# Kernel tuning notes

Hardware: AMD Instinct MI355X
Metric: run time of the kernel (lower is better)

The kernel has to match this reference:

```python
import jax, jax.numpy as jnp
import numpy as np

IN_CH = 256
MED_CH = IN_CH // 2


def setup_inputs() -> dict:
    key = jax.random.key(0)
    ks = jax.random.split(key, 9)
    B, C, H, W = 16, IN_CH, 64, 64
    s = 1.0 / np.sqrt(C)
    sm = 1.0 / np.sqrt(MED_CH)
    return {
        "x": jax.random.normal(ks[0], (B, C, H, W), dtype=jnp.float32),
        "w_o": jax.random.normal(ks[1], (MED_CH, C), dtype=jnp.float32) * s,
        "b_o": jax.random.normal(ks[2], (MED_CH,), dtype=jnp.float32) * 0.01,
        "w_v": jax.random.normal(ks[3], (MED_CH, C), dtype=jnp.float32) * s,
        "b_v": jax.random.normal(ks[4], (MED_CH,), dtype=jnp.float32) * 0.01,
        "w_c": jax.random.normal(ks[5], (C, MED_CH), dtype=jnp.float32) * sm,
        "b_c": jax.random.normal(ks[6], (C,), dtype=jnp.float32) * 0.01,
        "gamma": jax.random.normal(ks[7], (1,), dtype=jnp.float32) * 0.1,
    }


def reference(x, w_o, b_o, w_v, b_v, w_c, b_c, gamma):
    B, C, H, W = x.shape
    N = H * W
    xf = x.reshape(B, C, N)  # [B,C,N]
    # 1x1 convs == per-pixel linear projections
    o = jnp.einsum("mc,bcn->bmn", w_o, xf) + b_o[None, :, None]   # [B,M,N]
    v = jnp.einsum("mc,bcn->bmn", w_v, xf) + b_v[None, :, None]   # [B,M,N]
    x_o = o.transpose(0, 2, 1)                                     # [B,N,M]
    x_v = jax.nn.softmax(v, axis=-1)                               # softmax over N
    # NOTE: original code reuses conv_v for the 's' branch (conv_s unused)
    x_s = jax.nn.softmax(v.transpose(0, 2, 1), axis=-1)            # [B,N,M], softmax over M
    A = jnp.einsum("bmn,bnk->bmk", x_v, x_s)                       # [B,M,M]
    Bt = jnp.einsum("bnm,bmk->bnk", x_o, A).transpose(0, 2, 1)     # [B,M,N]
    out = jax.nn.relu(jnp.einsum("cm,bmn->bcn", w_c, Bt) + b_c[None, :, None])
    result = gamma[0] * out.reshape(B, C, H, W) + x
    return result
```

## Files before the change

kernel.cpp:

```cpp
#include <hip/hip_runtime.h>
#include <math.h>

constexpr int Bn = 16;
constexpr int Cn = 256;
constexpr int Mn = 128;
constexpr int Nn = 4096;

typedef short bf16x8 __attribute__((ext_vector_type(8)));
typedef float f32x4 __attribute__((ext_vector_type(4)));
typedef unsigned short us8 __attribute__((ext_vector_type(8)));
typedef unsigned short us4 __attribute__((ext_vector_type(4)));

static __device__ __forceinline__ unsigned short f2bf(float f) {
  union { float f; unsigned int u; } c{f};
  unsigned int u = c.u;
  u += 0x7FFFu + ((u >> 16) & 1u);
  return (unsigned short)(u >> 16);
}

static __device__ __forceinline__ void gload_lds16(const void* g, void* l) {
  __builtin_amdgcn_global_load_lds(
      (const __attribute__((address_space(1))) unsigned int*)g,
      (__attribute__((address_space(3))) unsigned int*)l, 16, 0, 0);
}

__global__ __launch_bounds__(256) void k_prep_w(
    const float* __restrict__ w_o, const float* __restrict__ w_v,
    unsigned short* __restrict__ Wv, unsigned short* __restrict__ woT,
    float* __restrict__ rs) {
  int idx = blockIdx.x * 256 + threadIdx.x;
  if (idx < Bn * Mn) rs[idx] = 0.f;
  if (idx < 8192) {
    int row = idx >> 6;
    int c4 = (idx & 63) * 4;
    float4 f = *(const float4*)&w_v[(size_t)row * Cn + c4];
    us4 g = {f2bf(f.x), f2bf(f.y), f2bf(f.z), f2bf(f.w)};
    *(us4*)&Wv[(size_t)row * Cn + c4] = g;
  } else {
    int j = idx - 8192;
    int cp = j >> 5;
    int m4 = (j & 31) * 4;
    us4 g;
#pragma unroll
    for (int e = 0; e < 4; ++e) g[e] = f2bf(w_o[(size_t)(m4 + e) * Cn + cp]);
    *(us4*)&woT[(size_t)cp * Mn + m4] = g;
  }
}

__global__ __launch_bounds__(256) void k_prep_x(
    const float* __restrict__ x, unsigned short* __restrict__ xT) {
  const int b = blockIdx.z;
  const int c0 = blockIdx.y * 128;
  const int n0 = blockIdx.x * 64;
  const int t = threadIdx.x;
  const int n4 = (t & 15) * 4;
  const int c8 = c0 + (t >> 4) * 8;
  const float* xb = x + ((size_t)b * Cn + c8) * Nn + n0 + n4;
  float4 r[8];
#pragma unroll
  for (int i = 0; i < 8; ++i) r[i] = *(const float4*)&xb[(size_t)i * Nn];
  unsigned short* dst = xT + ((size_t)b * Nn + n0 + n4) * Cn + c8;
#pragma unroll
  for (int j = 0; j < 4; ++j) {
    us8 g;
#pragma unroll
    for (int i = 0; i < 8; ++i) g[i] = f2bf(((const float*)&r[i])[j]);
    *(us8*)&dst[(size_t)j * Cn] = g;
  }
}

__global__ __launch_bounds__(256) void k_proj_v(
    const unsigned short* __restrict__ Wv,
    const unsigned short* __restrict__ xT,
    const float* __restrict__ b_v,
    float* __restrict__ Ap, float* __restrict__ rs) {
  __shared__ us8 pool[16 * 128 * 2];
  __shared__ float cs_lds[4][128];
  unsigned short* ldsA = (unsigned short*)pool;
  unsigned short* ldsB = (unsigned short*)pool + 8 * 128 * 8;
  const int b = blockIdx.y;
  const int nt = blockIdx.x;
  const int t = threadIdx.x;
  const int wave = t >> 6, lane = t & 63;
  const int quad = lane >> 4, l16 = lane & 15;
  const int wm = (wave & 1) * 64, wn = (wave >> 1) * 64;
  f32x4 acc[4][4] = {};
  const unsigned short* xb = xT + ((size_t)b * Nn + nt * 128) * Cn;
  const int rowS = t & 127;
  const int gS = t >> 7;

  uint4 rB[4];
#pragma unroll
  for (int p = 0; p < 4; ++p)
    rB[p] = *(const uint4*)&xb[(size_t)rowS * Cn + (p * 2 + gS) * 8];

  for (int k0 = 0; k0 < Cn; k0 += 64) {
#pragma unroll
    for (int p = 0; p < 4; ++p) {
      int s = p * 256 + t;
      *(uint4*)&ldsB[(size_t)s * 8] = rB[p];
      gload_lds16(&Wv[(size_t)rowS * Cn + k0 + (p * 2 + gS) * 8],
                  &ldsA[(size_t)s * 8]);
    }
    __syncthreads();
    if (k0 + 64 < Cn) {
#pragma unroll
      for (int p = 0; p < 4; ++p)
        rB[p] = *(const uint4*)&xb[(size_t)rowS * Cn + k0 + 64 + (p * 2 + gS) * 8];
    }
#pragma unroll
    for (int s = 0; s < 2; ++s) {
      bf16x8 af[4], bfr[4];
#pragma unroll
      for (int i = 0; i < 4; ++i)
        af[i] = *(const bf16x8*)&ldsA[(size_t)((s * 4 + quad) * 128 + wm + i * 16 + l16) * 8];
#pragma unroll
      for (int j = 0; j < 4; ++j)
        bfr[j] = *(const bf16x8*)&ldsB[(size_t)((s * 4 + quad) * 128 + wn + j * 16 + l16) * 8];
#pragma unroll
      for (int i = 0; i < 4; ++i)
#pragma unroll
        for (int j = 0; j < 4; ++j)
          acc[i][j] = __builtin_amdgcn_mfma_f32_16x16x32_bf16(af[i], bfr[j], acc[i][j], 0, 0, 0);
    }
    __syncthreads();
  }

#pragma unroll
  for (int i = 0; i < 4; ++i) {
#pragma unroll
    for (int r = 0; r < 4; ++r) {
      float bi = b_v[wm + i * 16 + quad * 4 + r];
#pragma unroll
      for (int j = 0; j < 4; ++j)
        acc[i][j][r] = __expf(acc[i][j][r] + bi);
    }
  }

#pragma unroll
  for (int i = 0; i < 4; ++i) {
#pragma unroll
    for (int r = 0; r < 4; ++r) {
      float s = acc[i][0][r] + acc[i][1][r] + acc[i][2][r] + acc[i][3][r];
      s += __shfl_xor(s, 1); s += __shfl_xor(s, 2);
      s += __shfl_xor(s, 4); s += __shfl_xor(s, 8);
      if (l16 == 0)
        atomicAdd(&rs[b * Mn + wm + i * 16 + quad * 4 + r], s);
    }
  }

  float csj[4];
#pragma unroll
  for (int j = 0; j < 4; ++j) {
    float c = 0.f;
#pragma unroll
    for (int i = 0; i < 4; ++i)
#pragma unroll
      for (int r = 0; r < 4; ++r) c += acc[i][j][r];
    c += __shfl_xor(c, 16);
    c += __shfl_xor(c, 32);
    csj[j] = c;
  }
  if (quad == 0) {
#pragma unroll
    for (int j = 0; j < 4; ++j) cs_lds[wave][wn + j * 16 + l16] = csj[j];
  }
  __syncthreads();

  const int cbase = (wave >> 1) * 2;
  float rinv[4];
#pragma unroll
  for (int j = 0; j < 4; ++j) {
    int nl = wn + j * 16 + l16;
    rinv[j] = rsqrtf(cs_lds[cbase][nl] + cs_lds[cbase + 1][nl]);
  }

  unsigned short* Hs = (unsigned short*)pool;
  unsigned short* Ls = Hs + 16 * 128 * 8;
#pragma unroll
  for (int i = 0; i < 4; ++i) {
#pragma unroll
    for (int r = 0; r < 4; ++r) {
      int m = wm + i * 16 + quad * 4 + r;
#pragma unroll
      for (int j = 0; j < 4; ++j) {
        int nl = wn + j * 16 + l16;
        float u = acc[i][j][r] * rinv[j];
        unsigned short h = f2bf(u);
        union { unsigned int q; float f; } hf{(unsigned int)h << 16};
        int idx = ((nl >> 3) * 128 + (m ^ (nl >> 3))) * 8 + (nl & 7);
        Hs[idx] = h;
        Ls[idx] = f2bf(u - hf.f);
      }
    }
  }
  __syncthreads();

  const bf16x8* Hv = (const bf16x8*)pool;
  const bf16x8* Lv = Hv + 16 * 128;
#pragma unroll
  for (int i = 0; i < 4; ++i)
#pragma unroll
    for (int j = 0; j < 4; ++j) acc[i][j] = (f32x4){0.f, 0.f, 0.f, 0.f};
#pragma unroll
  for (int s = 0; s < 4; ++s) {
    int g = s * 4 + quad;
    bf16x8 hA[4], lA[4], hB[4], lB[4];
#pragma unroll
    for (int i = 0; i < 4; ++i) {
      int mi = wm + i * 16 + l16;
      int ki = wn + i * 16 + l16;
      hA[i] = Hv[g * 128 + (mi ^ g)];
      lA[i] = Lv[g * 128 + (mi ^ g)];
      hB[i] = Hv[g * 128 + (ki ^ g)];
      lB[i] = Lv[g * 128 + (ki ^ g)];
    }
#pragma unroll
    for (int i = 0; i < 4; ++i)
#pragma unroll
      for (int j = 0; j < 4; ++j) {
        acc[i][j] = __builtin_amdgcn_mfma_f32_16x16x32_bf16(hA[i], hB[j], acc[i][j], 0, 0, 0);
        acc[i][j] = __builtin_amdgcn_mfma_f32_16x16x32_bf16(hA[i], lB[j], acc[i][j], 0, 0, 0);
        acc[i][j] = __builtin_amdgcn_mfma_f32_16x16x32_bf16(lA[i], hB[j], acc[i][j], 0, 0, 0);
      }
  }

  float* Apb = Ap + ((size_t)nt * Bn + b) * (Mn * Mn);
#pragma unroll
  for (int i = 0; i < 4; ++i) {
#pragma unroll
    for (int r = 0; r < 4; ++r) {
      int m = wm + i * 16 + quad * 4 + r;
      float* row = &Apb[(size_t)m * Mn];
#pragma unroll
      for (int j = 0; j < 4; ++j)
        row[wn + j * 16 + l16] = acc[i][j][r];
    }
  }
}

__global__ __launch_bounds__(256) void k_reduceA(
    const float* __restrict__ Ap, const float* __restrict__ rs,
    float* __restrict__ A, int S) {
  int tid = blockIdx.x * 256 + threadIdx.x;
  int idx4 = tid * 4;
  int b = idx4 / (Mn * Mn);
  int off = idx4 - b * (Mn * Mn);
  float4 s = {0.f, 0.f, 0.f, 0.f};
  for (int s0 = 0; s0 < S; ++s0) {
    float4 p = *(const float4*)&Ap[((size_t)s0 * Bn + b) * (Mn * Mn) + off];
    s.x += p.x; s.y += p.y; s.z += p.z; s.w += p.w;
  }
  float sc = 1.0f / rs[b * Mn + (off >> 7)];
  s.x *= sc; s.y *= sc; s.z *= sc; s.w *= sc;
  *(float4*)&A[idx4] = s;
}

__global__ __launch_bounds__(256) void k_w2(
    const float* __restrict__ w_c, const float* __restrict__ A,
    unsigned short* __restrict__ W2bf) {
  __shared__ float As[64][68];
  __shared__ float wcs[64][68];
  const int b = blockIdx.z;
  const int m0 = blockIdx.x * 64;
  const int c0 = blockIdx.y * 64;
  const int t = threadIdx.x;
  const int tc = (t >> 4) * 4, tmm = (t & 15) * 4;
  float acc[4][4] = {};
  for (int k0 = 0; k0 < Mn; k0 += 64) {
    int r = t >> 2;
    int k4 = (t & 3) * 4;
#pragma unroll
    for (int p = 0; p < 4; ++p) {
      int k = k4 + p * 16;
      float4 a4 = *(const float4*)&A[((size_t)(b * Mn + m0 + r)) * Mn + k0 + k];
      As[k + 0][r] = a4.x; As[k + 1][r] = a4.y; As[k + 2][r] = a4.z; As[k + 3][r] = a4.w;
      float4 w4 = *(const float4*)&w_c[(size_t)(c0 + r) * Mn + k0 + k];
      wcs[k + 0][r] = w4.x; wcs[k + 1][r] = w4.y; wcs[k + 2][r] = w4.z; wcs[k + 3][r] = w4.w;
    }
    __syncthreads();
#pragma unroll
    for (int kk = 0; kk < 64; ++kk) {
      float4 w4 = *(const float4*)&wcs[kk][tc];
      float4 a4 = *(const float4*)&As[kk][tmm];
      float w[4] = {w4.x, w4.y, w4.z, w4.w};
      float a[4] = {a4.x, a4.y, a4.z, a4.w};
#pragma unroll
      for (int i = 0; i < 4; ++i)
#pragma unroll
        for (int jj = 0; jj < 4; ++jj) acc[i][jj] = fmaf(w[i], a[jj], acc[i][jj]);
    }
    __syncthreads();
  }
#pragma unroll
  for (int i = 0; i < 4; ++i) {
    us4 g4 = {f2bf(acc[i][0]), f2bf(acc[i][1]), f2bf(acc[i][2]), f2bf(acc[i][3])};
    *(us4*)&W2bf[((size_t)(b * Cn + c0 + tc + i)) * Mn + m0 + tmm] = g4;
  }
}

__global__ __launch_bounds__(256) void k_ww(
    const unsigned short* __restrict__ W2bf, const unsigned short* __restrict__ woT,
    const float* __restrict__ b_o, const float* __restrict__ b_c,
    unsigned short* __restrict__ WW, float* __restrict__ bb) {
  __shared__ us8 ldsA[128 * 16];
  __shared__ us8 ldsB[128 * 16];
  __shared__ float bo_lds[128];
  const int b = blockIdx.z;
  const int c_t = blockIdx.y * 128;
  const int cp_t = blockIdx.x * 128;
  const int t = threadIdx.x;
  const int wave = t >> 6, lane = t & 63;
  const int quad = lane >> 4, l16 = lane & 15;
  const int wc = (wave & 1) * 64, wp = (wave >> 1) * 64;
  const unsigned short* W2b = W2bf + ((size_t)b * Cn + c_t) * Mn;
  const unsigned short* woB = woT + (size_t)cp_t * Mn;

#pragma unroll
  for (int p = 0; p < 8; ++p) {
    int s = p * 256 + t;
    int row = s >> 4, g = s & 15;
    int slot = row * 16 + (g ^ (row & 15));
    ldsA[slot] = *(const us8*)&W2b[(size_t)row * Mn + g * 8];
    ldsB[slot] = *(const us8*)&woB[(size_t)row * Mn + g * 8];
  }
  if (blockIdx.x == 0 && t < 128) bo_lds[t] = b_o[t];
  __syncthreads();

  f32x4 acc[4][4] = {};
#pragma unroll
  for (int s = 0; s < 4; ++s) {
    int gq = s * 4 + quad;
    int xo = gq ^ l16;
    bf16x8 af[4], bfr[4];
#pragma unroll
    for (int i = 0; i < 4; ++i)
      af[i] = *(const bf16x8*)&ldsA[(wc + i * 16 + l16) * 16 + xo];
#pragma unroll
    for (int j = 0; j < 4; ++j)
      bfr[j] = *(const bf16x8*)&ldsB[(wp + j * 16 + l16) * 16 + xo];
#pragma unroll
    for (int i = 0; i < 4; ++i)
#pragma unroll
      for (int j = 0; j < 4; ++j)
        acc[i][j] = __builtin_amdgcn_mfma_f32_16x16x32_bf16(af[i], bfr[j], acc[i][j], 0, 0, 0);
  }

#pragma unroll
  for (int i = 0; i < 4; ++i) {
#pragma unroll
    for (int r = 0; r < 4; ++r) {
      int c = c_t + wc + i * 16 + quad * 4 + r;
      unsigned short* row = &WW[((size_t)b * Cn + c) * Cn + cp_t];
#pragma unroll
      for (int j = 0; j < 4; ++j)
        row[wp + j * 16 + l16] = f2bf(acc[i][j][r]);
    }
  }

  if (blockIdx.x == 0 && t < 128) {
    float s = 0.f;
#pragma unroll
    for (int g = 0; g < 16; ++g) {
      us8 h = ldsA[t * 16 + (g ^ (t & 15))];
#pragma unroll
      for (int e = 0; e < 8; ++e) {
        union { unsigned int u; float f; } cv{(unsigned int)h[e] << 16};
        s = fmaf(cv.f, bo_lds[g * 8 + e], s);
      }
    }
    bb[b * Cn + c_t + t] = s + b_c[c_t + t];
  }
}

__global__ __launch_bounds__(256) void k_final_mfma(
    const unsigned short* __restrict__ WW, const unsigned short* __restrict__ xT,
    const float* __restrict__ x, const float* __restrict__ bb,
    const float* __restrict__ gamma, float* __restrict__ out) {
  __shared__ us8 ldsA[128 * 16];
  __shared__ us8 ldsB[128 * 16];
  const int b = blockIdx.z;
  const int c_t = blockIdx.y * 128;
  const int n_t = blockIdx.x * 128;
  const int t = threadIdx.x;
  const int wave = t >> 6, lane = t & 63;
  const int quad = lane >> 4, l16 = lane & 15;
  const int wc = (wave & 1) * 64, wn = (wave >> 1) * 64;
  const unsigned short* WWb = WW + ((size_t)b * Cn + c_t) * Cn;
  const unsigned short* xTb = xT + ((size_t)b * Nn + n_t) * Cn;

  f32x4 acc[4][4] = {};
  for (int k0 = 0; k0 < Cn; k0 += 128) {
#pragma unroll
    for (int p = 0; p < 8; ++p) {
      int s = p * 256 + t;
      int row = s >> 4, g = s & 15;
      int slot = row * 16 + (g ^ (row & 15));
      ldsA[slot] = *(const us8*)&WWb[(size_t)row * Cn + k0 + g * 8];
      ldsB[slot] = *(const us8*)&xTb[(size_t)row * Cn + k0 + g * 8];
    }
    __syncthreads();
#pragma unroll
    for (int s = 0; s < 4; ++s) {
      int gq = s * 4 + quad;
      int xo = gq ^ l16;
      bf16x8 af[4], bfr[4];
#pragma unroll
      for (int i = 0; i < 4; ++i)
        af[i] = *(const bf16x8*)&ldsA[(wc + i * 16 + l16) * 16 + xo];
#pragma unroll
      for (int j = 0; j < 4; ++j)
        bfr[j] = *(const bf16x8*)&ldsB[(wn + j * 16 + l16) * 16 + xo];
#pragma unroll
      for (int i = 0; i < 4; ++i)
#pragma unroll
        for (int j = 0; j < 4; ++j)
          acc[i][j] = __builtin_amdgcn_mfma_f32_16x16x32_bf16(af[i], bfr[j], acc[i][j], 0, 0, 0);
    }
    __syncthreads();
  }

  float g = gamma[0];
#pragma unroll
  for (int i = 0; i < 4; ++i) {
#pragma unroll
    for (int r = 0; r < 4; ++r) {
      int c = c_t + wc + i * 16 + quad * 4 + r;
      float bias = bb[b * Cn + c];
      const float* xr = &x[((size_t)b * Cn + c) * Nn + n_t];
      float* orow = &out[((size_t)b * Cn + c) * Nn + n_t];
#pragma unroll
      for (int j = 0; j < 4; ++j) {
        int n = wn + j * 16 + l16;
        orow[n] = g * fmaxf(acc[i][j][r] + bias, 0.f) + xr[n];
      }
    }
  }
}

extern "C" void kernel_launch(void* const* d_in, const int* in_sizes, int n_in,
                              void* d_out, int out_size, void* d_ws, size_t ws_size,
                              hipStream_t stream) {
  const float* x   = (const float*)d_in[0];
  const float* w_o = (const float*)d_in[1];
  const float* b_o = (const float*)d_in[2];
  const float* w_v = (const float*)d_in[3];
  const float* b_v = (const float*)d_in[4];
  const float* w_c = (const float*)d_in[5];
  const float* b_c = (const float*)d_in[6];
  const float* gm  = (const float*)d_in[7];

  constexpr int S = Nn / 128;
  float* ws = (float*)d_ws;
  float* rs = ws;
  float* bb = rs + Bn * Mn;
  float* A  = bb + Bn * Cn;
  float* Ap = A + (size_t)Bn * Mn * Mn;
  unsigned short* WW   = (unsigned short*)(Ap + (size_t)S * Bn * Mn * Mn);
  unsigned short* W2bf = WW + (size_t)Bn * Cn * Cn;
  unsigned short* xT   = W2bf + (size_t)Bn * Cn * Mn;
  unsigned short* Wv   = xT + (size_t)Bn * Nn * Cn;
  unsigned short* woT  = Wv + (size_t)Mn * Cn;

  k_prep_w<<<dim3(64), 256, 0, stream>>>(w_o, w_v, Wv, woT, rs);
  k_prep_x<<<dim3(Nn / 64, 2, Bn), 256, 0, stream>>>(x, xT);
  k_proj_v<<<dim3(Nn / 128, Bn), 256, 0, stream>>>(Wv, xT, b_v, Ap, rs);
  k_reduceA<<<dim3(Bn * Mn * Mn / 1024), 256, 0, stream>>>(Ap, rs, A, S);
  k_w2<<<dim3(Mn / 64, Cn / 64, Bn), 256, 0, stream>>>(w_c, A, W2bf);
  k_ww<<<dim3(2, 2, Bn), 256, 0, stream>>>(W2bf, woT, b_o, b_c, WW, bb);
  k_final_mfma<<<dim3(Nn / 128, Cn / 128, Bn), 256, 0, stream>>>(WW, xT, x, bb, gm, (float*)d_out);
}
```

Measured before the change: 210.2 us.

## Load MFMA operands directly from global memory and merge prep kernels

Both GEMM-style kernels (k_proj_v and k_final_mfma) drop LDS staging and barriers and now read bf16x8 MFMA fragments straight from global memory, relying on the cache for operand reuse across waves. The weight-prep and x-transpose kernels are merged into one launch, removing a kernel boundary. k_proj_v also gains a launch-bounds occupancy hint. The risk is more global/L2 traffic and uncoalesced 16-byte row-strided loads in place of shared-memory reuse.

```diff
diff --git a/kernel.cpp b/kernel.cpp
--- a/kernel.cpp
+++ b/kernel.cpp
@@ -18,41 +18,36 @@
   return (unsigned short)(u >> 16);
 }
 
-static __device__ __forceinline__ void gload_lds16(const void* g, void* l) {
-  __builtin_amdgcn_global_load_lds(
-      (const __attribute__((address_space(1))) unsigned int*)g,
-      (__attribute__((address_space(3))) unsigned int*)l, 16, 0, 0);
-}
-
-__global__ __launch_bounds__(256) void k_prep_w(
+__global__ __launch_bounds__(256) void k_prep(
+    const float* __restrict__ x, unsigned short* __restrict__ xT,
     const float* __restrict__ w_o, const float* __restrict__ w_v,
     unsigned short* __restrict__ Wv, unsigned short* __restrict__ woT,
     float* __restrict__ rs) {
-  int idx = blockIdx.x * 256 + threadIdx.x;
-  if (idx < Bn * Mn) rs[idx] = 0.f;
-  if (idx < 8192) {
-    int row = idx >> 6;
-    int c4 = (idx & 63) * 4;
-    float4 f = *(const float4*)&w_v[(size_t)row * Cn + c4];
-    us4 g = {f2bf(f.x), f2bf(f.y), f2bf(f.z), f2bf(f.w)};
-    *(us4*)&Wv[(size_t)row * Cn + c4] = g;
-  } else {
-    int j = idx - 8192;
-    int cp = j >> 5;
-    int m4 = (j & 31) * 4;
-    us4 g;
-#pragma unroll
-    for (int e = 0; e < 4; ++e) g[e] = f2bf(w_o[(size_t)(m4 + e) * Cn + cp]);
-    *(us4*)&woT[(size_t)cp * Mn + m4] = g;
-  }
-}
-
-__global__ __launch_bounds__(256) void k_prep_x(
-    const float* __restrict__ x, unsigned short* __restrict__ xT) {
   const int b = blockIdx.z;
   const int c0 = blockIdx.y * 128;
   const int n0 = blockIdx.x * 64;
   const int t = threadIdx.x;
+
+  if (blockIdx.y == 0 && blockIdx.z == 0) {
+    int idx = blockIdx.x * 256 + t;
+    if (idx < Bn * Mn) rs[idx] = 0.f;
+    if (idx < 8192) {
+      int row = idx >> 6;
+      int c4 = (idx & 63) * 4;
+      float4 f = *(const float4*)&w_v[(size_t)row * Cn + c4];
+      us4 g = {f2bf(f.x), f2bf(f.y), f2bf(f.z), f2bf(f.w)};
+      *(us4*)&Wv[(size_t)row * Cn + c4] = g;
+    } else {
+      int j = idx - 8192;
+      int cp = j >> 5;
+      int m4 = (j & 31) * 4;
+      us4 g;
+#pragma unroll
+      for (int e = 0; e < 4; ++e) g[e] = f2bf(w_o[(size_t)(m4 + e) * Cn + cp]);
+      *(us4*)&woT[(size_t)cp * Mn + m4] = g;
+    }
+  }
+
   const int n4 = (t & 15) * 4;
   const int c8 = c0 + (t >> 4) * 8;
   const float* xb = x + ((size_t)b * Cn + c8) * Nn + n0 + n4;
@@ -69,15 +64,13 @@
   }
 }
 
-__global__ __launch_bounds__(256) void k_proj_v(
+__global__ __launch_bounds__(256, 2) void k_proj_v(
     const unsigned short* __restrict__ Wv,
     const unsigned short* __restrict__ xT,
     const float* __restrict__ b_v,
     float* __restrict__ Ap, float* __restrict__ rs) {
   __shared__ us8 pool[16 * 128 * 2];
   __shared__ float cs_lds[4][128];
-  unsigned short* ldsA = (unsigned short*)pool;
-  unsigned short* ldsB = (unsigned short*)pool + 8 * 128 * 8;
   const int b = blockIdx.y;
   const int nt = blockIdx.x;
   const int t = threadIdx.x;
@@ -86,44 +79,22 @@
   const int wm = (wave & 1) * 64, wn = (wave >> 1) * 64;
   f32x4 acc[4][4] = {};
   const unsigned short* xb = xT + ((size_t)b * Nn + nt * 128) * Cn;
-  const int rowS = t & 127;
-  const int gS = t >> 7;
-
-  uint4 rB[4];
-#pragma unroll
-  for (int p = 0; p < 4; ++p)
-    rB[p] = *(const uint4*)&xb[(size_t)rowS * Cn + (p * 2 + gS) * 8];
-
-  for (int k0 = 0; k0 < Cn; k0 += 64) {
-#pragma unroll
-    for (int p = 0; p < 4; ++p) {
-      int s = p * 256 + t;
-      *(uint4*)&ldsB[(size_t)s * 8] = rB[p];
-      gload_lds16(&Wv[(size_t)rowS * Cn + k0 + (p * 2 + gS) * 8],
-                  &ldsA[(size_t)s * 8]);
-    }
-    __syncthreads();
-    if (k0 + 64 < Cn) {
-#pragma unroll
-      for (int p = 0; p < 4; ++p)
-        rB[p] = *(const uint4*)&xb[(size_t)rowS * Cn + k0 + 64 + (p * 2 + gS) * 8];
-    }
-#pragma unroll
-    for (int s = 0; s < 2; ++s) {
-      bf16x8 af[4], bfr[4];
-#pragma unroll
-      for (int i = 0; i < 4; ++i)
-        af[i] = *(const bf16x8*)&ldsA[(size_t)((s * 4 + quad) * 128 + wm + i * 16 + l16) * 8];
-#pragma unroll
-      for (int j = 0; j < 4; ++j)
-        bfr[j] = *(const bf16x8*)&ldsB[(size_t)((s * 4 + quad) * 128 + wn + j * 16 + l16) * 8];
-#pragma unroll
-      for (int i = 0; i < 4; ++i)
-#pragma unroll
-        for (int j = 0; j < 4; ++j)
-          acc[i][j] = __builtin_amdgcn_mfma_f32_16x16x32_bf16(af[i], bfr[j], acc[i][j], 0, 0, 0);
-    }
-    __syncthreads();
+
+#pragma unroll
+  for (int step = 0; step < 8; ++step) {
+    const int cc = step * 32 + quad * 8;
+    bf16x8 af[4], bfr[4];
+#pragma unroll
+    for (int i = 0; i < 4; ++i)
+      af[i] = *(const bf16x8*)&Wv[(size_t)(wm + i * 16 + l16) * Cn + cc];
+#pragma unroll
+    for (int j = 0; j < 4; ++j)
+      bfr[j] = *(const bf16x8*)&xb[(size_t)(wn + j * 16 + l16) * Cn + cc];
+#pragma unroll
+    for (int i = 0; i < 4; ++i)
+#pragma unroll
+      for (int j = 0; j < 4; ++j)
+        acc[i][j] = __builtin_amdgcn_mfma_f32_16x16x32_bf16(af[i], bfr[j], acc[i][j], 0, 0, 0);
   }
 
 #pragma unroll
@@ -377,8 +348,6 @@
     const unsigned short* __restrict__ WW, const unsigned short* __restrict__ xT,
     const float* __restrict__ x, const float* __restrict__ bb,
     const float* __restrict__ gamma, float* __restrict__ out) {
-  __shared__ us8 ldsA[128 * 16];
-  __shared__ us8 ldsB[128 * 16];
   const int b = blockIdx.z;
   const int c_t = blockIdx.y * 128;
   const int n_t = blockIdx.x * 128;
@@ -390,34 +359,21 @@
   const unsigned short* xTb = xT + ((size_t)b * Nn + n_t) * Cn;
 
   f32x4 acc[4][4] = {};
-  for (int k0 = 0; k0 < Cn; k0 += 128) {
-#pragma unroll
-    for (int p = 0; p < 8; ++p) {
-      int s = p * 256 + t;
-      int row = s >> 4, g = s & 15;
-      int slot = row * 16 + (g ^ (row & 15));
-      ldsA[slot] = *(const us8*)&WWb[(size_t)row * Cn + k0 + g * 8];
-      ldsB[slot] = *(const us8*)&xTb[(size_t)row * Cn + k0 + g * 8];
-    }
-    __syncthreads();
-#pragma unroll
-    for (int s = 0; s < 4; ++s) {
-      int gq = s * 4 + quad;
-      int xo = gq ^ l16;
-      bf16x8 af[4], bfr[4];
-#pragma unroll
-      for (int i = 0; i < 4; ++i)
-        af[i] = *(const bf16x8*)&ldsA[(wc + i * 16 + l16) * 16 + xo];
-#pragma unroll
-      for (int j = 0; j < 4; ++j)
-        bfr[j] = *(const bf16x8*)&ldsB[(wn + j * 16 + l16) * 16 + xo];
-#pragma unroll
-      for (int i = 0; i < 4; ++i)
-#pragma unroll
-        for (int j = 0; j < 4; ++j)
-          acc[i][j] = __builtin_amdgcn_mfma_f32_16x16x32_bf16(af[i], bfr[j], acc[i][j], 0, 0, 0);
-    }
-    __syncthreads();
+#pragma unroll
+  for (int step = 0; step < 8; ++step) {
+    const int cc = step * 32 + quad * 8;
+    bf16x8 af[4], bfr[4];
+#pragma unroll
+    for (int i = 0; i < 4; ++i)
+      af[i] = *(const bf16x8*)&WWb[(size_t)(wc + i * 16 + l16) * Cn + cc];
+#pragma unroll
+    for (int j = 0; j < 4; ++j)
+      bfr[j] = *(const bf16x8*)&xTb[(size_t)(wn + j * 16 + l16) * Cn + cc];
+#pragma unroll
+    for (int i = 0; i < 4; ++i)
+#pragma unroll
+      for (int j = 0; j < 4; ++j)
+        acc[i][j] = __builtin_amdgcn_mfma_f32_16x16x32_bf16(af[i], bfr[j], acc[i][j], 0, 0, 0);
   }
 
   float g = gamma[0];
@@ -462,8 +418,7 @@
   unsigned short* Wv   = xT + (size_t)Bn * Nn * Cn;
   unsigned short* woT  = Wv + (size_t)Mn * Cn;
 
-  k_prep_w<<<dim3(64), 256, 0, stream>>>(w_o, w_v, Wv, woT, rs);
-  k_prep_x<<<dim3(Nn / 64, 2, Bn), 256, 0, stream>>>(x, xT);
+  k_prep<<<dim3(Nn / 64, 2, Bn), 256, 0, stream>>>(x, xT, w_o, w_v, Wv, woT, rs);
   k_proj_v<<<dim3(Nn / 128, Bn), 256, 0, stream>>>(Wv, xT, b_v, Ap, rs);
   k_reduceA<<<dim3(Bn * Mn * Mn / 1024), 256, 0, stream>>>(Ap, rs, A, S);
   k_w2<<<dim3(Mn / 64, Cn / 64, Bn), 256, 0, stream>>>(w_c, A, W2bf);
```

Result: slower. 244.1 us (+16.1%).
